# Kernel tuning notes

Measured on AMD Instinct MI355X. Metric: run time of the kernel, lower is better.

The kernel has to match this reference:

```python
import jax, jax.numpy as jnp
import numpy as np

WEIGHT_BIT = 8
BIAS_BIT = 32
STRIDE = (1, 1)
PAD = ((1, 1), (1, 1))


def setup_inputs() -> dict:
    key = jax.random.key(0)
    k1, k2, k3, k4 = jax.random.split(key, 4)
    N, Cin, Cout, K, H, W = 64, 256, 256, 3, 28, 28
    x_q = jax.random.randint(k1, (N, Cin, H, W), 0, 255, dtype=jnp.int32)
    scale_x = jax.random.uniform(k2, (1,), dtype=jnp.float32) * 0.1 + 0.01
    weight = jax.random.normal(k3, (Cout, Cin, K, K), dtype=jnp.float32) * 0.05
    bias = jax.random.normal(k4, (Cout,), dtype=jnp.float32) * 0.1
    return {"x_q": x_q, "scale_x": scale_x, "weight": weight, "bias": bias}


def _quant_weight_per_channel(w, bit):
    # symmetric per-output-channel quantization from min/max (ZeroQ SymmetricQuantFunction)
    n = 2 ** (bit - 1) - 1  # 127 for 8-bit
    wf = w.reshape(w.shape[0], -1)
    sat = jnp.maximum(jnp.abs(wf.min(axis=1)), jnp.abs(wf.max(axis=1)))
    scale = jnp.clip(sat, 1e-8, None) / n  # [Cout]
    w_q = jnp.clip(jnp.round(w / scale[:, None, None, None]), -n - 1, n).astype(jnp.int32)
    return w_q, scale


def reference(x_q, scale_x, weight, bias):
    # fake-quantize weight per output channel
    w_q, scale_w = _quant_weight_per_channel(weight, WEIGHT_BIT)  # int32 [Cout,Cin,K,K], f32 [Cout]
    scale_out = scale_w * scale_x[0]  # [Cout]
    # quantize bias with the combined scale (bias_bit=32)
    nb = float(2 ** (BIAS_BIT - 1) - 1)
    b_q = jnp.clip(jnp.round(bias / scale_out), -nb - 1.0, nb).astype(jnp.int32)  # [Cout]
    out_q = jax.lax.conv_general_dilated(
        x_q, w_q, window_strides=STRIDE, padding=PAD,
        dimension_numbers=("NCHW", "OIHW", "NCHW"),
    ) + b_q[None, :, None, None]
    return out_q, scale_out.reshape(1, -1, 1, 1)
```

## Files before the change

kernel.cpp:

```cpp
#include <hip/hip_runtime.h>
#include <hip/hip_bf16.h>

typedef int   i32x4 __attribute__((ext_vector_type(4)));

#define N_IMG 64
#define CIN   256
#define COUT  256
#define HH    28
#define WW    28
#define PH    30
#define PW    30
#define M_TOT (N_IMG*HH*WW)
#define OUT_ELEMS (N_IMG*COUT*HH*WW)

#define XT_BYTES   ((size_t)N_IMG*PH*PW*CIN)
#define WT_OFF     (XT_BYTES)
#define WT_BYTES   ((size_t)9*COUT*CIN)
#define BQ_OFF     (WT_OFF + WT_BYTES)

#define GLD16(g, l) __builtin_amdgcn_global_load_lds( \
    (const __attribute__((address_space(1))) void*)(g), \
    (__attribute__((address_space(3))) void*)(l), 16, 0, 0)

__global__ __launch_bounds__(256) void transform_x(const int* __restrict__ xq,
                                                   signed char* __restrict__ xt) {
    __shared__ int xs[CIN*29];
    const int b = blockIdx.x;
    const int n = b / PH, py = b % PH;
    const int t = threadIdx.x;
    signed char* dst = xt + ((size_t)(n*PH + py))*PW*CIN;
    if (py == 0 || py == PH-1) {
        for (int i = t; i < PW*CIN; i += 256) dst[i] = -127;
        return;
    }
    const int h = py - 1;
    const int* src = xq + (size_t)n*CIN*HH*WW + h*WW;
    for (int i = t; i < CIN*WW; i += 256) {
        const int ci = i / WW, w = i % WW;
        xs[ci*29 + w] = src[ci*HH*WW + w];
    }
    __syncthreads();
    for (int i = t; i < PW*CIN; i += 256) {
        const int px = i / CIN, ci = i % CIN;
        const int v = (px == 0 || px == PW-1) ? 0 : xs[ci*29 + (px-1)];
        dst[px*CIN + ci] = (signed char)(v - 127);
    }
}

__global__ __launch_bounds__(256) void quant_w(const float* __restrict__ weight,
                                               const float* __restrict__ scale_x,
                                               const float* __restrict__ bias,
                                               signed char* __restrict__ wt,
                                               int* __restrict__ bq,
                                               float* __restrict__ out_tail) {
    __shared__ float red[256];
    __shared__ int  sred[256];
    const int co = blockIdx.x, t = threadIdx.x;
    const float* wrow = weight + (size_t)co*CIN*9;
    float wv[9];
    float mx = 0.f;
    for (int it = 0; it < 9; ++it) {
        float v = wrow[it*256 + t];
        wv[it] = v;
        mx = fmaxf(mx, fabsf(v));
    }
    red[t] = mx;
    __syncthreads();
    for (int s = 128; s > 0; s >>= 1) {
        if (t < s) red[t] = fmaxf(red[t], red[t+s]);
        __syncthreads();
    }
    const float scale = fmaxf(red[0], 1e-8f) / 127.f;
    int isum = 0;
    for (int it = 0; it < 9; ++it) {
        const int i = it*256 + t;
        const int ci = i / 9, rs = i % 9;
        float q = rintf(wv[it] / scale);
        q = fminf(fmaxf(q, -128.f), 127.f);
        const int qi = (int)q;
        isum += qi;
        wt[(size_t)rs*COUT*CIN + co*CIN + ci] = (signed char)qi;
    }
    sred[t] = isum;
    __syncthreads();
    for (int s = 128; s > 0; s >>= 1) {
        if (t < s) sred[t] += sred[t+s];
        __syncthreads();
    }
    if (t == 0) {
        const float so = scale * scale_x[0];
        out_tail[co] = so;
        bq[co] = (int)rintf(bias[co] / so) + 127 * sred[0];
    }
}

__global__ __launch_bounds__(256, 2) void conv_mfma(const signed char* __restrict__ xt,
                                                    const signed char* __restrict__ wt,
                                                    const int* __restrict__ bq,
                                                    float* __restrict__ out) {
    __shared__ signed char Ash[2*16384];
    __shared__ signed char Bsh[2*16384];
    const int d = threadIdx.x;
    const int w4 = d >> 6;
    const int lane = d & 63, lr = lane & 15, kg = lane >> 4;
    const int wm = w4 >> 1, wn = w4 & 1;
    const int bx = blockIdx.x;
    const int mb = (bx & 7)*49 + (bx >> 3);
    const int m0 = mb << 7;
    const int co0 = blockIdx.y << 7;

    const int srow = d >> 3;
    const int skc  = (d & 7) ^ (srow & 7);
    const signed char* aS = wt + (size_t)(co0 + srow)*CIN + (skc << 4);
    const signed char* bS[4];
#pragma unroll
    for (int j = 0; j < 4; ++j) {
        const int m = m0 + srow + j*32;
        const int n = m / 784, hw = m % 784, h = hw / 28, wq = hw % 28;
        bS[j] = xt + ((size_t)((n*PH + h)*PW + wq))*CIN + (skc << 4);
    }
    const int w4off = w4 << 10;

    i32x4 acc[4][4] = {};

    const int a0 = (wm*64 + lr)*128 + ((kg ^ (lr & 7)) << 4);
    const int b0 = (wn*64 + lr)*128 + ((kg ^ (lr & 7)) << 4);

#define STAGE(T_, P_) do { \
    const int tap_ = (T_) >> 1, c_ = (T_) & 1; \
    const int r3_ = (tap_*171) >> 9; \
    const int ao_ = tap_*(COUT*CIN) + (c_ << 7); \
    const int bo_ = ((r3_*PW + (tap_ - r3_*3)) << 8) + (c_ << 7); \
    GLD16(aS + ao_,         Ash + (P_)*16384 +         w4off); \
    GLD16(aS + ao_ +  8192, Ash + (P_)*16384 +  4096 + w4off); \
    GLD16(aS + ao_ + 16384, Ash + (P_)*16384 +  8192 + w4off); \
    GLD16(aS + ao_ + 24576, Ash + (P_)*16384 + 12288 + w4off); \
    GLD16(bS[0] + bo_,      Bsh + (P_)*16384 +         w4off); \
    GLD16(bS[1] + bo_,      Bsh + (P_)*16384 +  4096 + w4off); \
    GLD16(bS[2] + bo_,      Bsh + (P_)*16384 +  8192 + w4off); \
    GLD16(bS[3] + bo_,      Bsh + (P_)*16384 + 12288 + w4off); \
} while (0)

#define COMPUTE(P_) do { \
    const signed char* A_ = Ash + (P_)*16384; \
    const signed char* B_ = Bsh + (P_)*16384; \
    _Pragma("unroll") \
    for (int ks = 0; ks < 2; ++ks) { \
        const int ar = a0 ^ (ks << 6); \
        const int br = b0 ^ (ks << 6); \
        i32x4 af[4], bf[4]; \
        _Pragma("unroll") \
        for (int mr = 0; mr < 4; ++mr) \
            af[mr] = *(const i32x4*)&A_[ar + mr*2048]; \
        _Pragma("unroll") \
        for (int nr = 0; nr < 4; ++nr) \
            bf[nr] = *(const i32x4*)&B_[br + nr*2048]; \
        _Pragma("unroll") \
        for (int mr = 0; mr < 4; ++mr) \
            _Pragma("unroll") \
            for (int nr = 0; nr < 4; ++nr) \
                acc[mr][nr] = __builtin_amdgcn_mfma_i32_16x16x64_i8( \
                    af[mr], bf[nr], acc[mr][nr], 0, 0, 0); \
    } \
} while (0)

#define SYNCPT() do { \
    asm volatile("s_waitcnt vmcnt(0) lgkmcnt(0)" ::: "memory"); \
    __builtin_amdgcn_s_barrier(); \
    __builtin_amdgcn_sched_barrier(0); \
} while (0)

    STAGE(0, 0);
#pragma unroll 1
    for (int tt = 0; tt < 18; tt += 2) {
        SYNCPT();
        STAGE(tt + 1, 1);
        COMPUTE(0);
        SYNCPT();
        if (tt < 16) STAGE(tt + 2, 0);
        COMPUTE(1);
    }

#pragma unroll
    for (int nr = 0; nr < 4; ++nr) {
        const int mm = m0 + wn*64 + nr*16 + lr;
        const int nn = mm / 784, hw2 = mm % 784;
        float* orow = out + (size_t)nn*COUT*784 + hw2;
#pragma unroll
        for (int mr = 0; mr < 4; ++mr) {
            const int co = co0 + wm*64 + mr*16 + kg*4;
#pragma unroll
            for (int rg = 0; rg < 4; ++rg)
                orow[(size_t)(co + rg)*784] = (float)(acc[mr][nr][rg] + bq[co + rg]);
        }
    }
#undef STAGE
#undef COMPUTE
#undef SYNCPT
}

extern "C" void kernel_launch(void* const* d_in, const int* in_sizes, int n_in,
                              void* d_out, int out_size, void* d_ws, size_t ws_size,
                              hipStream_t stream) {
    const int*   xq      = (const int*)d_in[0];
    const float* scale_x = (const float*)d_in[1];
    const float* weight  = (const float*)d_in[2];
    const float* bias    = (const float*)d_in[3];
    float* out = (float*)d_out;

    signed char* xt = (signed char*)d_ws;
    signed char* wt = (signed char*)((char*)d_ws + WT_OFF);
    int*         bq = (int*)((char*)d_ws + BQ_OFF);

    hipLaunchKernelGGL(transform_x, dim3(N_IMG*PH), dim3(256), 0, stream, xq, xt);
    hipLaunchKernelGGL(quant_w, dim3(COUT), dim3(256), 0, stream,
                       weight, scale_x, bias, wt, bq, out + OUT_ELEMS);
    hipLaunchKernelGGL(conv_mfma, dim3(M_TOT/128, COUT/128), dim3(256), 0, stream,
                       xt, wt, bq, out);
}
```

Before: 73.13 us.

## Merge input transform and weight quant into one vectorized prep kernel

Combines the activation layout transform and the per-channel weight quantization into a single launch, assigning block ranges to each role. The activation path now reads rows with 16-byte vector loads and writes four packed int8 channels per 32-bit store instead of byte stores. The shared buffer is reused for the reduction scratch in weight blocks. This removes one launch and cuts store instruction count, at the cost of a 28-int stride in shared memory that may cause bank conflicts on the gather.

Measured after the change: 72.77 us. Within noise of the previous version (-0.5%).

```diff
diff --git a/kernel.cpp b/kernel.cpp
--- a/kernel.cpp
+++ b/kernel.cpp
@@ -2,6 +2,7 @@
 #include <hip/hip_bf16.h>
 
 typedef int   i32x4 __attribute__((ext_vector_type(4)));
+typedef int   int4v __attribute__((ext_vector_type(4)));
 
 #define N_IMG 64
 #define CIN   256
@@ -22,40 +23,54 @@
     (const __attribute__((address_space(1))) void*)(g), \
     (__attribute__((address_space(3))) void*)(l), 16, 0, 0)
 
-__global__ __launch_bounds__(256) void transform_x(const int* __restrict__ xq,
-                                                   signed char* __restrict__ xt) {
-    __shared__ int xs[CIN*29];
+__global__ __launch_bounds__(256) void prep(const int* __restrict__ xq,
+                                            const float* __restrict__ weight,
+                                            const float* __restrict__ scale_x,
+                                            const float* __restrict__ bias,
+                                            signed char* __restrict__ xt,
+                                            signed char* __restrict__ wt,
+                                            int* __restrict__ bq,
+                                            float* __restrict__ out_tail) {
+    __shared__ int xs[CIN*28];
     const int b = blockIdx.x;
-    const int n = b / PH, py = b % PH;
     const int t = threadIdx.x;
-    signed char* dst = xt + ((size_t)(n*PH + py))*PW*CIN;
-    if (py == 0 || py == PH-1) {
-        for (int i = t; i < PW*CIN; i += 256) dst[i] = -127;
+
+    if (b < N_IMG*PH) {
+        const int n = b / PH, py = b % PH;
+        signed char* dst = xt + ((size_t)(n*PH + py))*PW*CIN;
+        if (py == 0 || py == PH-1) {
+            int* d4 = (int*)dst;
+            for (int i = t; i < PW*CIN/4; i += 256) d4[i] = 0x81818181;
+            return;
+        }
+        const int h = py - 1;
+        const int* src = xq + (size_t)n*CIN*HH*WW + h*WW;
+        for (int i = t; i < CIN*7; i += 256) {
+            const int ci = i / 7, q = i % 7;
+            const int4v v = *(const int4v*)(src + ci*HH*WW + q*4);
+            *(int4v*)&xs[ci*28 + q*4] = v;
+        }
+        __syncthreads();
+        for (int i = t; i < PW*CIN/4; i += 256) {
+            const int px = i >> 6, ci0 = (i & 63) << 2;
+            unsigned int o;
+            if (px == 0 || px == PW-1) o = 0x81818181u;
+            else {
+                const int w = px - 1;
+                const unsigned int b0 = (unsigned char)(xs[(ci0    )*28 + w] - 127);
+                const unsigned int b1 = (unsigned char)(xs[(ci0 + 1)*28 + w] - 127);
+                const unsigned int b2 = (unsigned char)(xs[(ci0 + 2)*28 + w] - 127);
+                const unsigned int b3 = (unsigned char)(xs[(ci0 + 3)*28 + w] - 127);
+                o = b0 | (b1 << 8) | (b2 << 16) | (b3 << 24);
+            }
+            ((unsigned int*)dst)[i] = o;
+        }
         return;
     }
-    const int h = py - 1;
-    const int* src = xq + (size_t)n*CIN*HH*WW + h*WW;
-    for (int i = t; i < CIN*WW; i += 256) {
-        const int ci = i / WW, w = i % WW;
-        xs[ci*29 + w] = src[ci*HH*WW + w];
-    }
-    __syncthreads();
-    for (int i = t; i < PW*CIN; i += 256) {
-        const int px = i / CIN, ci = i % CIN;
-        const int v = (px == 0 || px == PW-1) ? 0 : xs[ci*29 + (px-1)];
-        dst[px*CIN + ci] = (signed char)(v - 127);
-    }
-}
-
-__global__ __launch_bounds__(256) void quant_w(const float* __restrict__ weight,
-                                               const float* __restrict__ scale_x,
-                                               const float* __restrict__ bias,
-                                               signed char* __restrict__ wt,
-                                               int* __restrict__ bq,
-                                               float* __restrict__ out_tail) {
-    __shared__ float red[256];
-    __shared__ int  sred[256];
-    const int co = blockIdx.x, t = threadIdx.x;
+
+    float* red  = (float*)xs;
+    int*   sred = (int*)xs + 256;
+    const int co = b - N_IMG*PH;
     const float* wrow = weight + (size_t)co*CIN*9;
     float wv[9];
     float mx = 0.f;
@@ -212,9 +227,8 @@
     signed char* wt = (signed char*)((char*)d_ws + WT_OFF);
     int*         bq = (int*)((char*)d_ws + BQ_OFF);
 
-    hipLaunchKernelGGL(transform_x, dim3(N_IMG*PH), dim3(256), 0, stream, xq, xt);
-    hipLaunchKernelGGL(quant_w, dim3(COUT), dim3(256), 0, stream,
-                       weight, scale_x, bias, wt, bq, out + OUT_ELEMS);
+    hipLaunchKernelGGL(prep, dim3(N_IMG*PH + COUT), dim3(256), 0, stream,
+                       xq, weight, scale_x, bias, xt, wt, bq, out + OUT_ELEMS);
     hipLaunchKernelGGL(conv_mfma, dim3(M_TOT/128, COUT/128), dim3(256), 0, stream,
                        xt, wt, bq, out);
 }
```
